# Optimization experiments

Measured on AMD Instinct MI355X. Metric: run time of the kernel, lower is better.

The kernel has to match this reference:

```python
import jax, jax.numpy as jnp
import numpy as np

SHAPE_ = 32          # sqrt(max_seq_len); seq positions form a SHAPE_ x SHAPE_ grid
N_HEADS = 8
BATCH = 8
SEQ_LEN = SHAPE_ * SHAPE_  # 1024
HEAD_DIM = 64


def _construct_bias(w_, s):
    """bias[..., j, i] = w_rolled[..., s - i - 1 + j]  -> (1, h, s, s).
    'full' base type: roll last axis left by one (concat of w[...,1:] and w[...,0])."""
    w_ = jnp.concatenate([w_[..., 1:], w_[..., :1]], axis=-1)  # (1, h, 2s-1)
    j = jnp.arange(s)
    i = jnp.arange(s)
    idx = (s - 1 - i)[None, :] + j[:, None]  # (s_j, s_i), values in [0, 2s-2]
    return w_[..., idx]  # (1, h, s, s), axes (..., j, i)


def setup_inputs() -> dict:
    key = jax.random.key(0)
    k1, k2 = jax.random.split(key)
    v = jax.random.normal(k1, (BATCH, SEQ_LEN, N_HEADS, HEAD_DIM), dtype=jnp.float32)
    # learned 1D bias base, length 2*SHAPE_-1 for 'full' base type
    w = jax.random.normal(k2, (1, N_HEADS, 2 * SHAPE_ - 1), dtype=jnp.float32)
    return {"v": v, "w": w}


def reference(v, w):
    s = SHAPE_
    b, L, h, d = v.shape
    bias = _construct_bias(w, s)  # (1, h, s, s)
    # x_ = bias[:, :, None, :, None, :], y_ = bias[:, :, :, None, :, None]
    # w2[., h, a, b, c, e] = bias[., h, b, e] + bias[., h, a, c]  -> (1, h, s, s, s, s)
    w2 = bias[:, :, None, :, None, :] + bias[:, :, :, None, :, None]
    w2 = w2.reshape(1, h, s * s, s * s)  # (1, h, L, L)
    # original: repeat w2 over batch then einsum('nlhd,nhlj->njhd', v, transpose(w2, [0,1,3,2]))
    # => pbv[n, j, h, d] = sum_l v[n, l, h, d] * w2[0, h, j, l]; broadcast instead of repeat.
    return jnp.einsum('nlhd,hjl->njhd', v, w2[0])
```

## Files before the change

### kernel.cpp

```cpp
#include <hip/hip_runtime.h>
#include <hip/hip_bf16.h>


#define S 32
#define HD4 128

__global__ __launch_bounds__(128) void reduce_kernel(
    const float4* __restrict__ v, float4* __restrict__ Vc,
    float4* __restrict__ Ve) {
  int block = blockIdx.x;
  int t = threadIdx.x;
  bool isVc = block < 256;
  int b2 = isVc ? block : block - 256;
  int n = b2 >> 5;
  int x = b2 & 31;
  const float4* base = v + (size_t)n * 1024 * HD4 + t;
  float4 acc = make_float4(0.f, 0.f, 0.f, 0.f);
  if (isVc) {
#pragma unroll
    for (int c = 0; c < 32; ++c) {
      float4 r = base[(size_t)(c * S + x) * HD4];
      acc.x += r.x; acc.y += r.y; acc.z += r.z; acc.w += r.w;
    }
    Vc[(size_t)b2 * HD4 + t] = acc;
  } else {
#pragma unroll
    for (int e = 0; e < 32; ++e) {
      float4 r = base[(size_t)(x * S + e) * HD4];
      acc.x += r.x; acc.y += r.y; acc.z += r.z; acc.w += r.w;
    }
    Ve[(size_t)b2 * HD4 + t] = acc;
  }
}

__global__ __launch_bounds__(256) void terms_kernel(
    const float* __restrict__ w,
    const float* __restrict__ Vc, const float* __restrict__ Ve,
    float* __restrict__ T1, float* __restrict__ T2) {
  __shared__ float bias_s[32][32];
  __shared__ float vc_s[32][64];
  __shared__ float ve_s[32][64];
  int nh = blockIdx.x;
  int n = nh >> 3, h = nh & 7;
  int t = threadIdx.x;

  for (int idx = t; idx < 1024; idx += 256) {
    int b = idx >> 5, e = idx & 31;
    int k = (32 + b - e) % 63;
    bias_s[b][e] = w[h * 63 + k];
  }
  for (int idx = t; idx < 512; idx += 256) {
    int e = idx >> 4, d4 = idx & 15;
    size_t g = ((size_t)(n * S + e) * 8 + h) * 16 + d4;
    float4 a = ((const float4*)Vc)[g];
    float4 b = ((const float4*)Ve)[g];
    vc_s[e][d4 * 4 + 0] = a.x; vc_s[e][d4 * 4 + 1] = a.y;
    vc_s[e][d4 * 4 + 2] = a.z; vc_s[e][d4 * 4 + 3] = a.w;
    ve_s[e][d4 * 4 + 0] = b.x; ve_s[e][d4 * 4 + 1] = b.y;
    ve_s[e][d4 * 4 + 2] = b.z; ve_s[e][d4 * 4 + 3] = b.w;
  }
  __syncthreads();

  int d = t & 63;
  int bg = t >> 6;
  for (int b = bg; b < 32; b += 4) {
    float a1 = 0.f, a2 = 0.f;
#pragma unroll
    for (int e = 0; e < 32; ++e) {
      a1 += bias_s[b][e] * vc_s[e][d];
      a2 += bias_s[b][e] * ve_s[e][d];
    }
    size_t g = (size_t)(n * S + b) * 512 + h * 64 + d;
    T1[g] = a1;
    T2[g] = a2;
  }
}

__global__ __launch_bounds__(256) void out_kernel(
    const float4* __restrict__ T1, const float4* __restrict__ T2,
    float4* __restrict__ out) {
  int idx = blockIdx.x * 256 + threadIdx.x;
  int d4 = idx & 15;
  int h  = (idx >> 4) & 7;
  int j  = (idx >> 7) & 1023;
  int n  = idx >> 17;
  int b = j & 31, a = j >> 5;
  float4 x = T1[((n * S + b) * 8 + h) * 16 + d4];
  float4 y = T2[((n * S + a) * 8 + h) * 16 + d4];
  out[idx] = make_float4(x.x + y.x, x.y + y.y, x.z + y.z, x.w + y.w);
}

extern "C" void kernel_launch(void* const* d_in, const int* in_sizes, int n_in,
                              void* d_out, int out_size, void* d_ws, size_t ws_size,
                              hipStream_t stream) {
  const float* v = (const float*)d_in[0];
  const float* w = (const float*)d_in[1];
  float* out = (float*)d_out;
  float* ws  = (float*)d_ws;

  float* Vc = ws;
  float* Ve = ws + 131072;
  float* T1 = ws + 262144;
  float* T2 = ws + 393216;

  reduce_kernel<<<512, 128, 0, stream>>>((const float4*)v, (float4*)Vc,
                                         (float4*)Ve);
  terms_kernel<<<64, 256, 0, stream>>>(w, Vc, Ve, T1, T2);
  out_kernel<<<4096, 256, 0, stream>>>((const float4*)T1, (const float4*)T2,
                                       (float4*)out);
}
```

Before: 80.22 us.

## Fuse bias-term GEMV and output broadcast-add into one kernel over more blocks

Merges the terms kernel and the output kernel into one kernel that computes T1 and a slice of T2 in shared memory and writes the output directly. This drops the round trip of T1/T2 through global memory and one launch. It also spreads the work over 1024 blocks instead of 64, so the small GEMV stage gets more parallelism. The cost is that each block recomputes the full T1 for its (n,h), which repeats that arithmetic 16 times.

```diff
diff --git a/kernel.cpp b/kernel.cpp
--- a/kernel.cpp
+++ b/kernel.cpp
@@ -1,5 +1,4 @@
 #include <hip/hip_runtime.h>
-#include <hip/hip_bf16.h>
 
 
 #define S 32
@@ -33,61 +32,65 @@
   }
 }
 
-__global__ __launch_bounds__(256) void terms_kernel(
+__global__ __launch_bounds__(256) void fused_kernel(
     const float* __restrict__ w,
     const float* __restrict__ Vc, const float* __restrict__ Ve,
-    float* __restrict__ T1, float* __restrict__ T2) {
+    float4* __restrict__ out) {
   __shared__ float bias_s[32][32];
   __shared__ float vc_s[32][64];
   __shared__ float ve_s[32][64];
-  int nh = blockIdx.x;
+  __shared__ float t1_s[32][68];
+  __shared__ float t2_s[2][68];
+
+  int blk = blockIdx.x;
+  int a0 = (blk & 15) << 1;
+  int nh = blk >> 4;
   int n = nh >> 3, h = nh & 7;
   int t = threadIdx.x;
 
   for (int idx = t; idx < 1024; idx += 256) {
     int b = idx >> 5, e = idx & 31;
-    int k = (32 + b - e) % 63;
-    bias_s[b][e] = w[h * 63 + k];
+    bias_s[b][e] = w[h * 63 + (32 + b - e) % 63];
   }
   for (int idx = t; idx < 512; idx += 256) {
     int e = idx >> 4, d4 = idx & 15;
     size_t g = ((size_t)(n * S + e) * 8 + h) * 16 + d4;
-    float4 a = ((const float4*)Vc)[g];
-    float4 b = ((const float4*)Ve)[g];
-    vc_s[e][d4 * 4 + 0] = a.x; vc_s[e][d4 * 4 + 1] = a.y;
-    vc_s[e][d4 * 4 + 2] = a.z; vc_s[e][d4 * 4 + 3] = a.w;
-    ve_s[e][d4 * 4 + 0] = b.x; ve_s[e][d4 * 4 + 1] = b.y;
-    ve_s[e][d4 * 4 + 2] = b.z; ve_s[e][d4 * 4 + 3] = b.w;
+    float4 A = ((const float4*)Vc)[g];
+    float4 B = ((const float4*)Ve)[g];
+    *(float4*)(&vc_s[e][d4 * 4]) = A;
+    *(float4*)(&ve_s[e][d4 * 4]) = B;
   }
   __syncthreads();
 
   int d = t & 63;
   int bg = t >> 6;
   for (int b = bg; b < 32; b += 4) {
-    float a1 = 0.f, a2 = 0.f;
+    float acc = 0.f;
 #pragma unroll
-    for (int e = 0; e < 32; ++e) {
-      a1 += bias_s[b][e] * vc_s[e][d];
-      a2 += bias_s[b][e] * ve_s[e][d];
+    for (int e = 0; e < 32; ++e) acc += bias_s[b][e] * vc_s[e][d];
+    t1_s[b][d] = acc;
+  }
+  if (bg < 2) {
+    float acc = 0.f;
+#pragma unroll
+    for (int c = 0; c < 32; ++c) acc += bias_s[a0 + bg][c] * ve_s[c][d];
+    t2_s[bg][d] = acc;
+  }
+  __syncthreads();
+
+#pragma unroll
+  for (int ar = 0; ar < 2; ++ar) {
+    int a = a0 + ar;
+#pragma unroll
+    for (int it = 0; it < 2; ++it) {
+      int idx = it * 256 + t;
+      int b = idx >> 4, d4 = idx & 15;
+      float4 x = *(const float4*)(&t1_s[b][d4 * 4]);
+      float4 y = *(const float4*)(&t2_s[ar][d4 * 4]);
+      out[((size_t)(n * 1024 + a * S + b) * 8 + h) * 16 + d4] =
+          make_float4(x.x + y.x, x.y + y.y, x.z + y.z, x.w + y.w);
     }
-    size_t g = (size_t)(n * S + b) * 512 + h * 64 + d;
-    T1[g] = a1;
-    T2[g] = a2;
   }
-}
-
-__global__ __launch_bounds__(256) void out_kernel(
-    const float4* __restrict__ T1, const float4* __restrict__ T2,
-    float4* __restrict__ out) {
-  int idx = blockIdx.x * 256 + threadIdx.x;
-  int d4 = idx & 15;
-  int h  = (idx >> 4) & 7;
-  int j  = (idx >> 7) & 1023;
-  int n  = idx >> 17;
-  int b = j & 31, a = j >> 5;
-  float4 x = T1[((n * S + b) * 8 + h) * 16 + d4];
-  float4 y = T2[((n * S + a) * 8 + h) * 16 + d4];
-  out[idx] = make_float4(x.x + y.x, x.y + y.y, x.z + y.z, x.w + y.w);
 }
 
 extern "C" void kernel_launch(void* const* d_in, const int* in_sizes, int n_in,
@@ -100,12 +103,8 @@
 
   float* Vc = ws;
   float* Ve = ws + 131072;
-  float* T1 = ws + 262144;
-  float* T2 = ws + 393216;
 
   reduce_kernel<<<512, 128, 0, stream>>>((const float4*)v, (float4*)Vc,
                                          (float4*)Ve);
-  terms_kernel<<<64, 256, 0, stream>>>(w, Vc, Ve, T1, T2);
-  out_kernel<<<4096, 256, 0, stream>>>((const float4*)T1, (const float4*)T2,
-                                       (float4*)out);
+  fused_kernel<<<1024, 256, 0, stream>>>(w, Vc, Ve, (float4*)out);
 }
```

Result: faster. 77.58 us (-3.3%).
